# Performance work log

Measured on AMD Instinct MI355X. Metric: run time of the kernel, lower is better.

The kernel has to match this reference:

```python
import jax, jax.numpy as jnp
import numpy as np

B, L, D_MODEL = 2, 4096, 768
D_STATE, D_CONV, EXPAND = 16, 4, 2
E = EXPAND * D_MODEL
LN_EPS = 1e-5


def setup_inputs() -> dict:
    key = jax.random.key(0)
    ks = jax.random.split(key, 8)
    s = lambda k, shape, scale: (jax.random.normal(k, shape, jnp.float32) * scale)
    return {
        "x": jax.random.normal(ks[0], (B, L, D_MODEL), jnp.float32),
        "ln_g": jnp.ones((D_MODEL,), jnp.float32),
        "ln_b": jnp.zeros((D_MODEL,), jnp.float32),
        "W_in": s(ks[1], (D_MODEL, E), 0.02), "b_in": jnp.zeros((E,), jnp.float32),
        "W_conv": s(ks[2], (E, 1, D_CONV), 0.1), "b_conv": jnp.zeros((E,), jnp.float32),
        "W_xp": s(ks[3], (E, D_STATE + D_MODEL), 0.02), "b_xp": jnp.zeros((D_STATE + D_MODEL,), jnp.float32),
        "W_dt": s(ks[4], (E, D_STATE), 0.02), "b_dt": jnp.zeros((D_STATE,), jnp.float32),
        "W_us": s(ks[5], (D_STATE, D_MODEL), 0.02), "b_us": jnp.zeros((D_MODEL,), jnp.float32),
        "W_out": s(ks[6], (E, D_MODEL), 0.02), "b_out": jnp.zeros((D_MODEL,), jnp.float32),
    }


def reference(x, ln_g, ln_b, W_in, b_in, W_conv, b_conv, W_xp, b_xp, W_dt, b_dt, W_us, b_us, W_out, b_out):
    Bsz, Ls, Dm = x.shape
    # LayerNorm
    mu = jnp.mean(x, axis=-1, keepdims=True)
    var = jnp.mean((x - mu) ** 2, axis=-1, keepdims=True)
    xn = (x - mu) * jax.lax.rsqrt(var + LN_EPS) * ln_g + ln_b
    # in projection
    x_in = xn @ W_in + b_in  # [B, L, E]
    # causal depthwise conv1d (torch pads d_conv-1 both sides then slices [:L] == left-pad only)
    xc = jnp.transpose(x_in, (0, 2, 1))  # [B, E, L]
    xc = jax.lax.conv_general_dilated(
        xc, W_conv, window_strides=(1,), padding=[(D_CONV - 1, 0)],
        dimension_numbers=("NCH", "OIH", "NCH"), feature_group_count=E,
    ) + b_conv[None, :, None]
    x_act = jax.nn.silu(jnpp := jnp.transpose(xc, (0, 2, 1)))  # [B, L, E]
    # projections for scan
    xd = x_act @ W_xp + b_xp
    xs, ds = xd[..., :Dm], xd[..., Dm:]           # [B,L,D], [B,L,N]
    dt = jax.nn.softplus(x_act @ W_dt + b_dt)      # [B,L,N], > 0
    a = jnp.exp(-dt)
    bterm = ds * jnp.exp(-dt / 2)
    # The original python loop is equivalent to: v_i = a_i v_{i-1} + b_i (standard scan),
    # followed by k = L-1-i extra applications of u := a_i u + b_i at each position i:
    #   u_i = a_i^k v_i + b_i * (1 - a_i^k) / (1 - a_i)
    def step(carry, ab):
        at, bt = ab
        v = at * carry + bt
        return v, v
    _, v = jax.lax.scan(step, jnp.zeros((Bsz, dt.shape[-1]), x.dtype),
                        (jnp.swapaxes(a, 0, 1), jnp.swapaxes(bterm, 0, 1)))
    v = jnp.swapaxes(v, 0, 1)  # [B, L, N]
    k = jnp.arange(Ls - 1, -1, -1, dtype=x.dtype)[None, :, None]
    denom = jnp.expm1(-dt)  # = -(1 - a), strictly negative since dt > 0
    denom = jnp.where(denom > -1e-30, -1e-30, denom)
    us = jnp.exp(-k * dt) * v + bterm * jnp.expm1(-k * dt) / denom
    # output path (dropout is identity in eval)
    y = xs + us @ W_us + b_us                      # [B, L, D]
    y = jnp.concatenate([y, x_act[..., Dm:]], axis=-1) @ W_out + b_out
    return y
```

## Files before the change

kernel.cpp:

```cpp
#include <hip/hip_runtime.h>
#include <hip/hip_bf16.h>
#include <hip/hip_fp16.h>

#define B_SZ 2
#define L_SZ 4096
#define DM 768
#define DSt 16
#define E_SZ 1536
#define M_SZ (B_SZ*L_SZ)
#define NXD 800
#define NXD_PAD 896
#define LN_EPSF 1e-5f

typedef _Float16 h16;
typedef __attribute__((ext_vector_type(8))) _Float16 half8;
typedef __attribute__((ext_vector_type(4))) float f32x4;

__device__ inline void gload_lds16(const void* g, void* l) {
  __builtin_amdgcn_global_load_lds((const __attribute__((address_space(1))) unsigned int*)g,
                                   (__attribute__((address_space(3))) unsigned int*)l,
                                   16, 0, 0);
}

__global__ void wprep_kernel(const float* __restrict__ W_in, const float* __restrict__ W_xp,
                             const float* __restrict__ W_dt, const float* __restrict__ W_out,
                             const float* __restrict__ b_xp, const float* __restrict__ b_dt,
                             h16* __restrict__ Wt_in, h16* __restrict__ Wt_cat,
                             h16* __restrict__ Wt_out, float* __restrict__ bcat) {
  const int S1 = E_SZ * DM;
  const int S2 = NXD_PAD * E_SZ;
  const int S3 = DM * E_SZ;
  const int total = S1 + S2 + S3 + NXD;
  for (int idx = blockIdx.x * 256 + threadIdx.x; idx < total; idx += gridDim.x * 256) {
    if (idx < S1) {
      int n = idx / DM, k = idx % DM;
      Wt_in[idx] = (h16)W_in[(size_t)k * E_SZ + n];
    } else if (idx < S1 + S2) {
      int t = idx - S1;
      int n = t / E_SZ, k = t % E_SZ;
      float v = 0.f;
      if (n < 784)      v = W_xp[(size_t)k * 784 + n];
      else if (n < NXD) v = W_dt[(size_t)k * DSt + (n - 784)];
      Wt_cat[t] = (h16)v;
    } else if (idx < S1 + S2 + S3) {
      int t = idx - S1 - S2;
      int n = t / E_SZ, k = t % E_SZ;
      Wt_out[t] = (h16)W_out[(size_t)k * DM + n];
    } else {
      int c = idx - S1 - S2 - S3;
      bcat[c] = (c < 784) ? b_xp[c] : b_dt[c - 784];
    }
  }
}

__global__ void ln_kernel(const float* __restrict__ x, const float* __restrict__ g,
                          const float* __restrict__ beta, h16* __restrict__ xn) {
  int m = blockIdx.x;
  const float* row = x + (size_t)m * DM;
  float s = 0.f, ss = 0.f;
  for (int i = threadIdx.x; i < DM; i += 256) {
    float v = row[i];
    s += v; ss += v * v;
  }
  for (int d = 32; d; d >>= 1) { s += __shfl_down(s, d); ss += __shfl_down(ss, d); }
  __shared__ float red0[4], red1[4];
  int wid = threadIdx.x >> 6;
  if ((threadIdx.x & 63) == 0) { red0[wid] = s; red1[wid] = ss; }
  __syncthreads();
  __shared__ float sh_mu, sh_inv;
  if (threadIdx.x == 0) {
    s  = red0[0] + red0[1] + red0[2] + red0[3];
    ss = red1[0] + red1[1] + red1[2] + red1[3];
    float mu = s * (1.f / DM);
    float var = ss * (1.f / DM) - mu * mu;
    sh_mu = mu;
    sh_inv = rsqrtf(var + LN_EPSF);
  }
  __syncthreads();
  float mu = sh_mu, inv = sh_inv;
  h16* orow = xn + (size_t)m * DM;
  for (int i = threadIdx.x; i < DM; i += 256) {
    orow[i] = (h16)((row[i] - mu) * inv * g[i] + beta[i]);
  }
}

template <typename OutT>
__global__ __launch_bounds__(256)
void gemm_f16(const h16* __restrict__ A, int lda,
              const h16* __restrict__ A2, int lda2, int ksplit,
              const h16* __restrict__ Bt, int ldb,
              const float* __restrict__ bias,
              OutT* __restrict__ C, int ldc,
              int Nreal, int K) {
  __shared__ h16 Ash[128][32];
  __shared__ h16 Bsh[128][32];
  int tid = threadIdx.x;
  int w = tid >> 6, l = tid & 63;
  int m0 = blockIdx.y * 128;
  int n0 = blockIdx.x * 128;
  int wr = w >> 1, wc = w & 1;
  int lrow = l >> 2;
  int lcol = (l & 3) * 8;
  int fr = l & 15, fq = l >> 4;
  f32x4 acc[4][4] = {};

  for (int k0 = 0; k0 < K; k0 += 32) {
    const h16* Ap = (k0 >= ksplit) ? A2 : A;
    int ldA = (k0 >= ksplit) ? lda2 : lda;
    gload_lds16(Ap + (size_t)(m0 + 16 * w + lrow) * ldA + k0 + lcol,      &Ash[16 * w][0]);
    gload_lds16(Ap + (size_t)(m0 + 64 + 16 * w + lrow) * ldA + k0 + lcol, &Ash[64 + 16 * w][0]);
    gload_lds16(Bt + (size_t)(n0 + 16 * w + lrow) * ldb + k0 + lcol,      &Bsh[16 * w][0]);
    gload_lds16(Bt + (size_t)(n0 + 64 + 16 * w + lrow) * ldb + k0 + lcol, &Bsh[64 + 16 * w][0]);
    __syncthreads();
    half8 af[4], bf[4];
#pragma unroll
    for (int i = 0; i < 4; ++i)
      af[i] = *(const half8*)&Ash[wr * 64 + i * 16 + fr][fq * 8];
#pragma unroll
    for (int j = 0; j < 4; ++j)
      bf[j] = *(const half8*)&Bsh[wc * 64 + j * 16 + fr][fq * 8];
#pragma unroll
    for (int i = 0; i < 4; ++i)
#pragma unroll
      for (int j = 0; j < 4; ++j)
        acc[i][j] = __builtin_amdgcn_mfma_f32_16x16x32_f16(af[i], bf[j], acc[i][j], 0, 0, 0);
    __syncthreads();
  }
#pragma unroll
  for (int i = 0; i < 4; ++i) {
#pragma unroll
    for (int j = 0; j < 4; ++j) {
      int n = n0 + wc * 64 + j * 16 + fr;
      if (n < Nreal) {
        float b = bias[n];
#pragma unroll
        for (int r = 0; r < 4; ++r) {
          int m = m0 + wr * 64 + i * 16 + fq * 4 + r;
          C[(size_t)m * ldc + n] = (OutT)(acc[i][j][r] + b);
        }
      }
    }
  }
}

__global__ void conv_silu_kernel(const h16* __restrict__ x_in, const float* __restrict__ Wc,
                                 const float* __restrict__ bc, h16* __restrict__ x_act) {
  int idx = blockIdx.x * 256 + threadIdx.x;
  const int E8 = E_SZ / 8;
  if (idx >= M_SZ * E8) return;
  int e8 = idx % E8;
  int m = idx / E8;
  int t = m % L_SZ;
  int e0 = e8 * 8;
  const h16* p0 = x_in + (size_t)m * E_SZ + e0;
  half8 r0 = *(const half8*)p0;
  half8 r1 = {}, r2 = {}, r3 = {};
  if (t >= 1) r1 = *(const half8*)(p0 - E_SZ);
  if (t >= 2) r2 = *(const half8*)(p0 - 2 * E_SZ);
  if (t >= 3) r3 = *(const half8*)(p0 - 3 * E_SZ);
  half8 out;
#pragma unroll
  for (int j = 0; j < 8; ++j) {
    int e = e0 + j;
    float4 wv = *reinterpret_cast<const float4*>(&Wc[e * 4]);
    float acc = bc[e] + (float)r0[j] * wv.w + (float)r1[j] * wv.z
              + (float)r2[j] * wv.y + (float)r3[j] * wv.x;
    float sg = 1.f / (1.f + expf(-acc));
    out[j] = (h16)(acc * sg);
  }
  *(half8*)(x_act + (size_t)m * E_SZ + e0) = out;
}

__global__ void post_kernel(const h16* __restrict__ xd, float* __restrict__ dt_a,
                            float* __restrict__ a_a, float* __restrict__ bt_a) {
  int idx = blockIdx.x * 256 + threadIdx.x;
  if (idx >= M_SZ * DSt) return;
  int m = idx >> 4, s = idx & 15;
  float pre = (float)xd[(size_t)m * NXD + 784 + s];
  float dsv = (float)xd[(size_t)m * NXD + 768 + s];
  float dt = (pre > 20.f) ? pre : log1pf(expf(pre));
  dt_a[idx] = dt;
  a_a[idx] = expf(-dt);
  bt_a[idx] = dsv * expf(-0.5f * dt);
}

__global__ void scan_kernel(const float* __restrict__ a_a, const float* __restrict__ bt_a,
                            float* __restrict__ v_a) {
  int chain = blockIdx.x;
  int b = chain >> 4, s = chain & 15;
  int lane = threadIdx.x;
  const int CS = L_SZ / 64;
  size_t base = ((size_t)b * L_SZ + (size_t)lane * CS) * DSt + s;
  float A = 1.f, Bc = 0.f;
  for (int i = 0; i < CS; ++i) {
    float at = a_a[base + (size_t)i * DSt];
    float bt = bt_a[base + (size_t)i * DSt];
    Bc = fmaf(at, Bc, bt);
    A *= at;
  }
  for (int d = 1; d < 64; d <<= 1) {
    float Ao = __shfl_up(A, d);
    float Bo = __shfl_up(Bc, d);
    if (lane >= d) { Bc = fmaf(A, Bo, Bc); A *= Ao; }
  }
  float P = __shfl_up(Bc, 1);
  if (lane == 0) P = 0.f;
  float v = P;
  for (int i = 0; i < CS; ++i) {
    float at = a_a[base + (size_t)i * DSt];
    float bt = bt_a[base + (size_t)i * DSt];
    v = fmaf(at, v, bt);
    v_a[base + (size_t)i * DSt] = v;
  }
}

__global__ void us_y1_kernel(const h16* __restrict__ xd, const float* __restrict__ dt_a,
                             const float* __restrict__ bt_a, const float* __restrict__ v_a,
                             const float* __restrict__ W_us, const float* __restrict__ b_us,
                             h16* __restrict__ y1) {
  int m = blockIdx.x;
  int t = m % L_SZ;
  __shared__ float us_sh[DSt];
  if (threadIdx.x < DSt) {
    int s = threadIdx.x;
    float dt = dt_a[m * DSt + s];
    float v  = v_a[m * DSt + s];
    float bt = bt_a[m * DSt + s];
    float kk = (float)(L_SZ - 1 - t);
    float e1 = expf(-kk * dt);
    float em = expm1f(-kk * dt);
    float den = expm1f(-dt);
    if (den > -1e-30f) den = -1e-30f;
    us_sh[s] = e1 * v + bt * em / den;
  }
  __syncthreads();
  for (int n = threadIdx.x; n < DM; n += 256) {
    float acc = (float)xd[(size_t)m * NXD + n] + b_us[n];
#pragma unroll
    for (int k = 0; k < DSt; ++k)
      acc = fmaf(us_sh[k], W_us[k * DM + n], acc);
    y1[(size_t)m * DM + n] = (h16)acc;
  }
}

extern "C" void kernel_launch(void* const* d_in, const int* in_sizes, int n_in,
                              void* d_out, int out_size, void* d_ws, size_t ws_size,
                              hipStream_t stream) {
  const float* x      = (const float*)d_in[0];
  const float* ln_g   = (const float*)d_in[1];
  const float* ln_b   = (const float*)d_in[2];
  const float* W_in   = (const float*)d_in[3];
  const float* b_in   = (const float*)d_in[4];
  const float* W_conv = (const float*)d_in[5];
  const float* b_conv = (const float*)d_in[6];
  const float* W_xp   = (const float*)d_in[7];
  const float* b_xp   = (const float*)d_in[8];
  const float* W_dt   = (const float*)d_in[9];
  const float* b_dt   = (const float*)d_in[10];
  const float* W_us   = (const float*)d_in[11];
  const float* b_us   = (const float*)d_in[12];
  const float* W_out  = (const float*)d_in[13];
  const float* b_out  = (const float*)d_in[14];
  float* out = (float*)d_out;

  char* ws = (char*)d_ws;
  size_t off = 0;
  auto alloc = [&](size_t bytes) { void* p = ws + off; off = (off + bytes + 255) & ~(size_t)255; return p; };
  h16*   xn     = (h16*)alloc((size_t)M_SZ * DM * 2);
  h16*   x_in   = (h16*)alloc((size_t)M_SZ * E_SZ * 2);
  h16*   x_act  = (h16*)alloc((size_t)M_SZ * E_SZ * 2);
  h16*   xd     = (h16*)alloc((size_t)M_SZ * NXD * 2);
  h16*   y1     = (h16*)alloc((size_t)M_SZ * DM * 2);
  h16*   Wt_in  = (h16*)alloc((size_t)E_SZ * DM * 2);
  h16*   Wt_cat = (h16*)alloc((size_t)NXD_PAD * E_SZ * 2);
  h16*   Wt_out = (h16*)alloc((size_t)DM * E_SZ * 2);
  float* bcat   = (float*)alloc(NXD * 4);
  float* dt_a   = (float*)alloc((size_t)M_SZ * DSt * 4);
  float* a_a    = (float*)alloc((size_t)M_SZ * DSt * 4);
  float* bt_a   = (float*)alloc((size_t)M_SZ * DSt * 4);
  float* v_a    = (float*)alloc((size_t)M_SZ * DSt * 4);

  hipLaunchKernelGGL(wprep_kernel, dim3(8192), dim3(256), 0, stream,
                     W_in, W_xp, W_dt, W_out, b_xp, b_dt, Wt_in, Wt_cat, Wt_out, bcat);
  hipLaunchKernelGGL(ln_kernel, dim3(M_SZ), dim3(256), 0, stream, x, ln_g, ln_b, xn);
  hipLaunchKernelGGL((gemm_f16<h16>), dim3(E_SZ / 128, M_SZ / 128), dim3(256), 0, stream,
                     xn, DM, xn, DM, 1 << 30,
                     Wt_in, DM, b_in, x_in, E_SZ, E_SZ, DM);
  hipLaunchKernelGGL(conv_silu_kernel, dim3((M_SZ * E_SZ / 8) / 256), dim3(256), 0, stream,
                     x_in, W_conv, b_conv, x_act);
  hipLaunchKernelGGL((gemm_f16<h16>), dim3(NXD_PAD / 128, M_SZ / 128), dim3(256), 0, stream,
                     x_act, E_SZ, x_act, E_SZ, 1 << 30,
                     Wt_cat, E_SZ, bcat, xd, NXD, NXD, E_SZ);
  hipLaunchKernelGGL(post_kernel, dim3((M_SZ * DSt) / 256), dim3(256), 0, stream,
                     xd, dt_a, a_a, bt_a);
  hipLaunchKernelGGL(scan_kernel, dim3(B_SZ * DSt), dim3(64), 0, stream, a_a, bt_a, v_a);
  hipLaunchKernelGGL(us_y1_kernel, dim3(M_SZ), dim3(256), 0, stream,
                     xd, dt_a, bt_a, v_a, W_us, b_us, y1);
  hipLaunchKernelGGL((gemm_f16<float>), dim3(DM / 128, M_SZ / 128), dim3(256), 0, stream,
                     y1, DM, x_act, E_SZ, DM,
                     Wt_out, E_SZ, b_out, out, DM, DM, E_SZ);
}
```

Measured before the change: 336.3 us.

## Fold xs and us projections into output GEMM via precomputed combined weights

Uses linearity to precompute W_xp[:, :768] @ W_out[:768] and W_us @ W_out[:768] into one combined weight matrix, so the output GEMM reads x_act plus the padded us directly. This removes the wide 800-column xd GEMM and the y1 intermediate. The remaining dt/ds projection becomes a narrow 32-column GEMM, and softplus, scan and the us formula are fused into one kernel. Weight transposes now use a tiled LDS transpose. Extra per-call weight-prep GEMMs are added, and folding the weights in fp16 changes rounding.

```diff
diff --git a/kernel.cpp b/kernel.cpp
--- a/kernel.cpp
+++ b/kernel.cpp
@@ -8,8 +8,7 @@
 #define DSt 16
 #define E_SZ 1536
 #define M_SZ (B_SZ*L_SZ)
-#define NXD 800
-#define NXD_PAD 896
+#define KF 1568
 #define LN_EPSF 1e-5f
 
 typedef _Float16 h16;
@@ -22,35 +21,72 @@
                                    16, 0, 0);
 }
 
-__global__ void wprep_kernel(const float* __restrict__ W_in, const float* __restrict__ W_xp,
-                             const float* __restrict__ W_dt, const float* __restrict__ W_out,
+__global__ void wprep_kernel(const float* __restrict__ W_xp, const float* __restrict__ W_dt,
                              const float* __restrict__ b_xp, const float* __restrict__ b_dt,
-                             h16* __restrict__ Wt_in, h16* __restrict__ Wt_cat,
-                             h16* __restrict__ Wt_out, float* __restrict__ bcat) {
-  const int S1 = E_SZ * DM;
-  const int S2 = NXD_PAD * E_SZ;
-  const int S3 = DM * E_SZ;
-  const int total = S1 + S2 + S3 + NXD;
+                             h16* __restrict__ W_xp_h, h16* __restrict__ WsmT,
+                             float* __restrict__ bsm) {
+  const int S1 = E_SZ * 784;
+  const int S2 = 128 * E_SZ;
+  const int total = S1 + S2 + 32;
   for (int idx = blockIdx.x * 256 + threadIdx.x; idx < total; idx += gridDim.x * 256) {
     if (idx < S1) {
-      int n = idx / DM, k = idx % DM;
-      Wt_in[idx] = (h16)W_in[(size_t)k * E_SZ + n];
+      W_xp_h[idx] = (h16)W_xp[idx];
     } else if (idx < S1 + S2) {
       int t = idx - S1;
       int n = t / E_SZ, k = t % E_SZ;
       float v = 0.f;
-      if (n < 784)      v = W_xp[(size_t)k * 784 + n];
-      else if (n < NXD) v = W_dt[(size_t)k * DSt + (n - 784)];
-      Wt_cat[t] = (h16)v;
-    } else if (idx < S1 + S2 + S3) {
-      int t = idx - S1 - S2;
-      int n = t / E_SZ, k = t % E_SZ;
-      Wt_out[t] = (h16)W_out[(size_t)k * DM + n];
+      if (n < 16)      v = W_xp[(size_t)k * 784 + 768 + n];
+      else if (n < 32) v = W_dt[(size_t)k * DSt + (n - 16)];
+      WsmT[t] = (h16)v;
     } else {
-      int c = idx - S1 - S2 - S3;
-      bcat[c] = (c < 784) ? b_xp[c] : b_dt[c - 784];
+      int c = idx - S1 - S2;
+      bsm[c] = (c < 16) ? b_xp[768 + c] : b_dt[c - 16];
     }
   }
+}
+
+__global__ void transpose_f16_kernel(const float* __restrict__ src, int R, int C,
+                                     h16* __restrict__ dst, int ldd, int coff, int add) {
+  __shared__ h16 tile[64][65];
+  int r0 = blockIdx.y * 64, c0 = blockIdx.x * 64;
+  int lane = threadIdx.x & 63, grp = threadIdx.x >> 6;
+#pragma unroll
+  for (int i = 0; i < 16; ++i) {
+    int r = grp + i * 4;
+    tile[r][lane] = (h16)src[(size_t)(r0 + r) * C + c0 + lane];
+  }
+  __syncthreads();
+#pragma unroll
+  for (int i = 0; i < 16; ++i) {
+    int c = grp + i * 4;
+    size_t di = (size_t)(c0 + c) * ldd + coff + r0 + lane;
+    h16 v = tile[lane][c];
+    if (add) dst[di] = (h16)((float)dst[di] + (float)v);
+    else dst[di] = v;
+  }
+}
+
+__global__ void wcomb_kernel(const float* __restrict__ W_us, const float* __restrict__ W_out,
+                             const float* __restrict__ b_us, const float* __restrict__ b_xp,
+                             const float* __restrict__ b_out,
+                             h16* __restrict__ W_bigT, float* __restrict__ b_final) {
+  int n = blockIdx.x * 64 + (threadIdx.x & 63);
+  int sy = threadIdx.x >> 6;
+  float acc[4] = {};
+  float bacc = 0.f;
+  for (int j = 0; j < DM; ++j) {
+    float wv = W_out[(size_t)j * DM + n];
+#pragma unroll
+    for (int i = 0; i < 4; ++i) acc[i] += W_us[(sy * 4 + i) * DM + j] * wv;
+    if (sy == 0) bacc += (b_us[j] + b_xp[j]) * wv;
+  }
+#pragma unroll
+  for (int i = 0; i < 4; ++i) {
+    int s = sy * 4 + i;
+    W_bigT[(size_t)n * KF + 1536 + s] = (h16)acc[i];
+    W_bigT[(size_t)n * KF + 1552 + s] = (h16)0.f;
+  }
+  if (sy == 0) b_final[n] = b_out[n] + bacc;
 }
 
 __global__ void ln_kernel(const float* __restrict__ x, const float* __restrict__ g,
@@ -87,7 +123,7 @@
 template <typename OutT>
 __global__ __launch_bounds__(256)
 void gemm_f16(const h16* __restrict__ A, int lda,
-              const h16* __restrict__ A2, int lda2, int ksplit,
+              const h16* __restrict__ A2, int lda2, int ksplit, int k2off,
               const h16* __restrict__ Bt, int ldb,
               const float* __restrict__ bias,
               OutT* __restrict__ C, int ldc,
@@ -105,10 +141,11 @@
   f32x4 acc[4][4] = {};
 
   for (int k0 = 0; k0 < K; k0 += 32) {
-    const h16* Ap = (k0 >= ksplit) ? A2 : A;
-    int ldA = (k0 >= ksplit) ? lda2 : lda;
-    gload_lds16(Ap + (size_t)(m0 + 16 * w + lrow) * ldA + k0 + lcol,      &Ash[16 * w][0]);
-    gload_lds16(Ap + (size_t)(m0 + 64 + 16 * w + lrow) * ldA + k0 + lcol, &Ash[64 + 16 * w][0]);
+    const h16* Ap; int ldA; int kb;
+    if (k0 >= ksplit) { Ap = A2; ldA = lda2; kb = k0 - k2off; }
+    else              { Ap = A;  ldA = lda;  kb = k0; }
+    gload_lds16(Ap + (size_t)(m0 + 16 * w + lrow) * ldA + kb + lcol,      &Ash[16 * w][0]);
+    gload_lds16(Ap + (size_t)(m0 + 64 + 16 * w + lrow) * ldA + kb + lcol, &Ash[64 + 16 * w][0]);
     gload_lds16(Bt + (size_t)(n0 + 16 * w + lrow) * ldb + k0 + lcol,      &Bsh[16 * w][0]);
     gload_lds16(Bt + (size_t)(n0 + 64 + 16 * w + lrow) * ldb + k0 + lcol, &Bsh[64 + 16 * w][0]);
     __syncthreads();
@@ -132,7 +169,7 @@
     for (int j = 0; j < 4; ++j) {
       int n = n0 + wc * 64 + j * 16 + fr;
       if (n < Nreal) {
-        float b = bias[n];
+        float b = bias ? bias[n] : 0.f;
 #pragma unroll
         for (int r = 0; r < 4; ++r) {
           int m = m0 + wr * 64 + i * 16 + fq * 4 + r;
@@ -171,75 +208,54 @@
   *(half8*)(x_act + (size_t)m * E_SZ + e0) = out;
 }
 
-__global__ void post_kernel(const h16* __restrict__ xd, float* __restrict__ dt_a,
-                            float* __restrict__ a_a, float* __restrict__ bt_a) {
-  int idx = blockIdx.x * 256 + threadIdx.x;
-  if (idx >= M_SZ * DSt) return;
-  int m = idx >> 4, s = idx & 15;
-  float pre = (float)xd[(size_t)m * NXD + 784 + s];
-  float dsv = (float)xd[(size_t)m * NXD + 768 + s];
-  float dt = (pre > 20.f) ? pre : log1pf(expf(pre));
-  dt_a[idx] = dt;
-  a_a[idx] = expf(-dt);
-  bt_a[idx] = dsv * expf(-0.5f * dt);
-}
-
-__global__ void scan_kernel(const float* __restrict__ a_a, const float* __restrict__ bt_a,
-                            float* __restrict__ v_a) {
+__global__ void scan_fused_kernel(const float* __restrict__ sd, h16* __restrict__ us_pad) {
   int chain = blockIdx.x;
   int b = chain >> 4, s = chain & 15;
-  int lane = threadIdx.x;
-  const int CS = L_SZ / 64;
-  size_t base = ((size_t)b * L_SZ + (size_t)lane * CS) * DSt + s;
+  int t = threadIdx.x;
+  int mloc0 = t * 16;
+  size_t gbase = ((size_t)b * L_SZ + mloc0) * 32;
+  float dtv[16], av[16], btv[16];
   float A = 1.f, Bc = 0.f;
-  for (int i = 0; i < CS; ++i) {
-    float at = a_a[base + (size_t)i * DSt];
-    float bt = bt_a[base + (size_t)i * DSt];
-    Bc = fmaf(at, Bc, bt);
-    A *= at;
-  }
+#pragma unroll
+  for (int i = 0; i < 16; ++i) {
+    float pre = sd[gbase + (size_t)i * 32 + 16 + s];
+    float dsv = sd[gbase + (size_t)i * 32 + s];
+    float d = (pre > 20.f) ? pre : log1pf(expf(pre));
+    dtv[i] = d;
+    float a = expf(-d);
+    av[i] = a;
+    float bb = dsv * expf(-0.5f * d);
+    btv[i] = bb;
+    Bc = fmaf(a, Bc, bb);
+    A *= a;
+  }
+  int lane = t & 63, w = t >> 6;
   for (int d = 1; d < 64; d <<= 1) {
-    float Ao = __shfl_up(A, d);
-    float Bo = __shfl_up(Bc, d);
+    float Ao = __shfl_up(A, d), Bo = __shfl_up(Bc, d);
     if (lane >= d) { Bc = fmaf(A, Bo, Bc); A *= Ao; }
   }
-  float P = __shfl_up(Bc, 1);
-  if (lane == 0) P = 0.f;
-  float v = P;
-  for (int i = 0; i < CS; ++i) {
-    float at = a_a[base + (size_t)i * DSt];
-    float bt = bt_a[base + (size_t)i * DSt];
-    v = fmaf(at, v, bt);
-    v_a[base + (size_t)i * DSt] = v;
-  }
-}
-
-__global__ void us_y1_kernel(const h16* __restrict__ xd, const float* __restrict__ dt_a,
-                             const float* __restrict__ bt_a, const float* __restrict__ v_a,
-                             const float* __restrict__ W_us, const float* __restrict__ b_us,
-                             h16* __restrict__ y1) {
-  int m = blockIdx.x;
-  int t = m % L_SZ;
-  __shared__ float us_sh[DSt];
-  if (threadIdx.x < DSt) {
-    int s = threadIdx.x;
-    float dt = dt_a[m * DSt + s];
-    float v  = v_a[m * DSt + s];
-    float bt = bt_a[m * DSt + s];
-    float kk = (float)(L_SZ - 1 - t);
-    float e1 = expf(-kk * dt);
-    float em = expm1f(-kk * dt);
-    float den = expm1f(-dt);
+  __shared__ float wA[4], wB[4];
+  if (lane == 63) { wA[w] = A; wB[w] = Bc; }
+  __syncthreads();
+  float pA = 1.f, pB = 0.f;
+  for (int i = 0; i < 4; ++i)
+    if (i < w) { pB = fmaf(wA[i], pB, wB[i]); pA *= wA[i]; }
+  float eA = __shfl_up(A, 1), eB = __shfl_up(Bc, 1);
+  if (lane == 0) { eA = 1.f; eB = 0.f; }
+  float v = fmaf(eA, pB, eB);
+#pragma unroll
+  for (int i = 0; i < 16; ++i) {
+    v = fmaf(av[i], v, btv[i]);
+    float d = dtv[i];
+    float kk = (float)(L_SZ - 1 - (mloc0 + i));
+    float e1 = expf(-kk * d);
+    float em = expm1f(-kk * d);
+    float den = expm1f(-d);
     if (den > -1e-30f) den = -1e-30f;
-    us_sh[s] = e1 * v + bt * em / den;
-  }
-  __syncthreads();
-  for (int n = threadIdx.x; n < DM; n += 256) {
-    float acc = (float)xd[(size_t)m * NXD + n] + b_us[n];
-#pragma unroll
-    for (int k = 0; k < DSt; ++k)
-      acc = fmaf(us_sh[k], W_us[k * DM + n], acc);
-    y1[(size_t)m * DM + n] = (h16)acc;
+    float us = fmaf(e1, v, btv[i] * em / den);
+    size_t gm = (size_t)b * L_SZ + mloc0 + i;
+    us_pad[gm * 32 + s] = (h16)us;
+    us_pad[gm * 32 + 16 + s] = (h16)0.f;
   }
 }
 
@@ -266,37 +282,44 @@
   char* ws = (char*)d_ws;
   size_t off = 0;
   auto alloc = [&](size_t bytes) { void* p = ws + off; off = (off + bytes + 255) & ~(size_t)255; return p; };
-  h16*   xn     = (h16*)alloc((size_t)M_SZ * DM * 2);
-  h16*   x_in   = (h16*)alloc((size_t)M_SZ * E_SZ * 2);
-  h16*   x_act  = (h16*)alloc((size_t)M_SZ * E_SZ * 2);
-  h16*   xd     = (h16*)alloc((size_t)M_SZ * NXD * 2);
-  h16*   y1     = (h16*)alloc((size_t)M_SZ * DM * 2);
-  h16*   Wt_in  = (h16*)alloc((size_t)E_SZ * DM * 2);
-  h16*   Wt_cat = (h16*)alloc((size_t)NXD_PAD * E_SZ * 2);
-  h16*   Wt_out = (h16*)alloc((size_t)DM * E_SZ * 2);
-  float* bcat   = (float*)alloc(NXD * 4);
-  float* dt_a   = (float*)alloc((size_t)M_SZ * DSt * 4);
-  float* a_a    = (float*)alloc((size_t)M_SZ * DSt * 4);
-  float* bt_a   = (float*)alloc((size_t)M_SZ * DSt * 4);
-  float* v_a    = (float*)alloc((size_t)M_SZ * DSt * 4);
-
-  hipLaunchKernelGGL(wprep_kernel, dim3(8192), dim3(256), 0, stream,
-                     W_in, W_xp, W_dt, W_out, b_xp, b_dt, Wt_in, Wt_cat, Wt_out, bcat);
+  h16*   xn      = (h16*)alloc((size_t)M_SZ * DM * 2);
+  h16*   x_in    = (h16*)alloc((size_t)M_SZ * E_SZ * 2);
+  h16*   x_act   = (h16*)alloc((size_t)M_SZ * E_SZ * 2);
+  float* sd      = (float*)alloc((size_t)M_SZ * 32 * 4);
+  h16*   us_pad  = (h16*)alloc((size_t)M_SZ * 32 * 2);
+  h16*   Wt_in   = (h16*)alloc((size_t)E_SZ * DM * 2);
+  h16*   Wt_out  = (h16*)alloc((size_t)DM * E_SZ * 2);
+  h16*   W_xp_h  = (h16*)alloc((size_t)E_SZ * 784 * 2);
+  h16*   WsmT    = (h16*)alloc((size_t)128 * E_SZ * 2);
+  h16*   W_bigT  = (h16*)alloc((size_t)DM * KF * 2);
+  float* bsm     = (float*)alloc(32 * 4);
+  float* b_final = (float*)alloc(DM * 4);
+
+  hipLaunchKernelGGL(wprep_kernel, dim3(4096), dim3(256), 0, stream,
+                     W_xp, W_dt, b_xp, b_dt, W_xp_h, WsmT, bsm);
+  hipLaunchKernelGGL(transpose_f16_kernel, dim3(E_SZ / 64, DM / 64), dim3(256), 0, stream,
+                     W_in, DM, E_SZ, Wt_in, DM, 0, 0);
+  hipLaunchKernelGGL(transpose_f16_kernel, dim3(DM / 64, E_SZ / 64), dim3(256), 0, stream,
+                     W_out, E_SZ, DM, Wt_out, E_SZ, 0, 0);
+  hipLaunchKernelGGL(wcomb_kernel, dim3(DM / 64), dim3(256), 0, stream,
+                     W_us, W_out, b_us, b_xp, b_out, W_bigT, b_final);
+  hipLaunchKernelGGL((gemm_f16<h16>), dim3(E_SZ / 128, DM / 128), dim3(256), 0, stream,
+                     Wt_out, E_SZ, Wt_out, E_SZ, 1 << 30, 0,
+                     W_xp_h, 784, (const float*)nullptr, W_bigT, KF, E_SZ, DM);
+  hipLaunchKernelGGL(transpose_f16_kernel, dim3(DM / 64, DM / 64), dim3(256), 0, stream,
+                     W_out + (size_t)DM * DM, DM, DM, W_bigT, KF, DM, 1);
+
   hipLaunchKernelGGL(ln_kernel, dim3(M_SZ), dim3(256), 0, stream, x, ln_g, ln_b, xn);
   hipLaunchKernelGGL((gemm_f16<h16>), dim3(E_SZ / 128, M_SZ / 128), dim3(256), 0, stream,
-                     xn, DM, xn, DM, 1 << 30,
+                     xn, DM, xn, DM, 1 << 30, 0,
                      Wt_in, DM, b_in, x_in, E_SZ, E_SZ, DM);
   hipLaunchKernelGGL(conv_silu_kernel, dim3((M_SZ * E_SZ / 8) / 256), dim3(256), 0, stream,
                      x_in, W_conv, b_conv, x_act);
-  hipLaunchKernelGGL((gemm_f16<h16>), dim3(NXD_PAD / 128, M_SZ / 128), dim3(256), 0, stream,
-                     x_act, E_SZ, x_act, E_SZ, 1 << 30,
-                     Wt_cat, E_SZ, bcat, xd, NXD, NXD, E_SZ);
-  hipLaunchKernelGGL(post_kernel, dim3((M_SZ * DSt) / 256), dim3(256), 0, stream,
-                     xd, dt_a, a_a, bt_a);
-  hipLaunchKernelGGL(scan_kernel, dim3(B_SZ * DSt), dim3(64), 0, stream, a_a, bt_a, v_a);
-  hipLaunchKernelGGL(us_y1_kernel, dim3(M_SZ), dim3(256), 0, stream,
-                     xd, dt_a, bt_a, v_a, W_us, b_us, y1);
+  hipLaunchKernelGGL((gemm_f16<float>), dim3(1, M_SZ / 128), dim3(256), 0, stream,
+                     x_act, E_SZ, x_act, E_SZ, 1 << 30, 0,
+                     WsmT, E_SZ, bsm, sd, 32, 32, E_SZ);
+  hipLaunchKernelGGL(scan_fused_kernel, dim3(B_SZ * DSt), dim3(256), 0, stream, sd, us_pad);
   hipLaunchKernelGGL((gemm_f16<float>), dim3(DM / 128, M_SZ / 128), dim3(256), 0, stream,
-                     y1, DM, x_act, E_SZ, DM,
-                     Wt_out, E_SZ, b_out, out, DM, DM, E_SZ);
-}
+                     x_act, E_SZ, us_pad, 32, E_SZ, E_SZ,
+                     W_bigT, KF, b_final, out, DM, DM, KF);
+}
```

Measured after the change: 452.9 us. 34.7% more time.
